# Optimization experiments

Hardware: AMD Instinct MI355X
Metric: run time of the kernel (lower is better)

The kernel has to match this reference:

```python
import jax, jax.numpy as jnp
import numpy as np

N_NODES = 100000
N_EDGES = 1600000
IN_CH, HID, OUT_CH = 256, 128, 40
NUM_LAYERS = 8
ALPHA = 0.5
THETA = 1.0


def setup_inputs() -> dict:
    key = jax.random.key(0)
    ks = jax.random.split(key, 8)
    x = jax.random.normal(ks[0], (N_NODES, IN_CH), dtype=jnp.float32)
    edge_index = jax.random.randint(ks[1], (2, N_EDGES), 0, N_NODES, dtype=jnp.int64)
    s1 = 1.0 / np.sqrt(IN_CH)
    s2 = 1.0 / np.sqrt(HID)
    lin1_w = jax.random.uniform(ks[2], (IN_CH, HID), jnp.float32, -s1, s1)
    lin1_b = jax.random.uniform(ks[3], (HID,), jnp.float32, -s1, s1)
    conv_ws = jax.random.uniform(ks[4], (NUM_LAYERS, HID, HID), jnp.float32, -s2, s2)
    lin2_w = jax.random.uniform(ks[5], (HID, OUT_CH), jnp.float32, -s2, s2)
    lin2_b = jax.random.uniform(ks[6], (OUT_CH,), jnp.float32, -s2, s2)
    return {"x": x, "edge_index": edge_index, "lin1_w": lin1_w, "lin1_b": lin1_b,
            "conv_ws": conv_ws, "lin2_w": lin2_w, "lin2_b": lin2_b}


def reference(x, edge_index, lin1_w, lin1_b, conv_ws, lin2_w, lin2_b):
    # Eval mode: dropout is identity. GCN2Conv with shared_weights=True:
    #   h_agg = A_hat @ h ; h = (1-alpha)*h_agg + alpha*x0
    #   out  = (1-beta)*h + beta*(h @ W_l), beta = log(theta/l + 1)
    n = x.shape[0]
    loops = jnp.arange(n, dtype=edge_index.dtype)
    row = jnp.concatenate([edge_index[0], loops])  # source
    col = jnp.concatenate([edge_index[1], loops])  # target (aggregation)
    deg = jax.ops.segment_sum(jnp.ones(row.shape[0], dtype=x.dtype), col, num_segments=n)
    dinv = jnp.where(deg > 0, deg ** -0.5, 0.0)
    enorm = dinv[row] * dinv[col]  # symmetric GCN normalization, [E+N]

    h = jax.nn.relu(x @ lin1_w + lin1_b)  # [N, HID]
    x0 = h
    for l in range(NUM_LAYERS):
        beta = float(np.log(THETA / (l + 1) + 1.0))
        agg = jax.ops.segment_sum(h[row] * enorm[:, None], col, num_segments=n)
        hc = (1.0 - ALPHA) * agg + ALPHA * x0
        h = jax.nn.relu((1.0 - beta) * hc + beta * (hc @ conv_ws[l]))
    out = h @ lin2_w + lin2_b
    return jax.nn.log_softmax(out, axis=1)
```

## Files before the change

kernel.cpp:

```cpp
#include <hip/hip_runtime.h>
#include <math.h>

#define NN 100000
#define NE 1600000
#define HID 128
#define INCH 256
#define OUTC 40
#define NLAYERS 8
#define NBUCK 391
#define EPB 4096
#define CAP 6144
#define LW 136

typedef __attribute__((ext_vector_type(8))) short bf16x8;
typedef __attribute__((ext_vector_type(4))) float f32x4;
typedef __attribute__((ext_vector_type(2))) float f32x2;

static __device__ inline unsigned short f2bf(float f) {
  unsigned u = __float_as_uint(f);
  unsigned r = (u + 0x7fff + ((u >> 16) & 1)) >> 16;
  return (unsigned short)r;
}
static __device__ inline float bflo(unsigned u) { return __uint_as_float(u << 16); }
static __device__ inline float bfhi(unsigned u) { return __uint_as_float(u & 0xffff0000u); }
static __device__ inline unsigned char f2fp8(float f) {
  return (unsigned char)(__builtin_amdgcn_cvt_pk_fp8_f32(f, f, 0, false) & 0xff);
}


static __global__ void k_zerob(int* __restrict__ bcnt, int* __restrict__ dbin) {
  int i = blockIdx.x * 256 + threadIdx.x;
  if (i < NBUCK) bcnt[i] = 0;
  if (i < 64) dbin[i] = 0;
}

static __global__ __launch_bounds__(256) void k_bhist(const int* __restrict__ ei,
                                                      int* __restrict__ bcnt) {
  __shared__ int lh[NBUCK + 1];
  int t = threadIdx.x;
  for (int i = t; i <= NBUCK; i += 256) lh[i] = 0;
  __syncthreads();
  int e0 = blockIdx.x * EPB;
  for (int k = t; k < EPB; k += 256) {
    int e = e0 + k;
    if (e < NE) atomicAdd(&lh[ei[NE + e] >> 8], 1);
  }
  __syncthreads();
  for (int i = t; i < NBUCK; i += 256)
    if (lh[i]) atomicAdd(&bcnt[i], lh[i]);
}

static __global__ void k_bscan(const int* __restrict__ bcnt, int* __restrict__ boffs,
                               int* __restrict__ bcur, int* __restrict__ offs) {
  __shared__ int sd[512];
  int t = threadIdx.x;
  sd[t] = (t < NBUCK) ? bcnt[t] : 0;
  __syncthreads();
  for (int d = 1; d < 512; d <<= 1) {
    int v = (t >= d) ? sd[t - d] : 0;
    __syncthreads();
    sd[t] += v;
    __syncthreads();
  }
  if (t < NBUCK) {
    boffs[t + 1] = sd[t];
    bcur[t] = sd[t] - bcnt[t];
  }
  if (t == 0) { boffs[0] = 0; offs[NN] = NE; }
}

static __global__ __launch_bounds__(256) void k_sortA(const int* __restrict__ ei,
                                                      int* __restrict__ bcur,
                                                      int2* __restrict__ stage) {
  __shared__ int lsrc[EPB], ldst[EPB];
  __shared__ int lh[NBUCK + 1], lbase[NBUCK + 1], lcur[NBUCK + 1];
  int t = threadIdx.x;
  int e0 = blockIdx.x * EPB;
  for (int k = t; k < EPB; k += 256) {
    int e = e0 + k;
    lsrc[k] = (e < NE) ? ei[e] : -1;
    ldst[k] = (e < NE) ? ei[NE + e] : -1;
  }
  for (int i = t; i <= NBUCK; i += 256) lh[i] = 0;
  __syncthreads();
  for (int k = t; k < EPB; k += 256)
    if (ldst[k] >= 0) atomicAdd(&lh[ldst[k] >> 8], 1);
  __syncthreads();
  for (int i = t; i < NBUCK; i += 256) {
    int c = lh[i];
    lbase[i] = c ? atomicAdd(&bcur[i], c) : 0;
    lcur[i] = 0;
  }
  __syncthreads();
  for (int k = t; k < EPB; k += 256) {
    int d = ldst[k];
    if (d >= 0) {
      int bu = d >> 8;
      int r = atomicAdd(&lcur[bu], 1);
      stage[lbase[bu] + r] = make_int2(lsrc[k], d);
    }
  }
}

static __global__ __launch_bounds__(256) void k_degs(
    const int2* __restrict__ stage, const int* __restrict__ boffs,
    int* __restrict__ offs, float* __restrict__ dinv, int* __restrict__ cursor,
    int* __restrict__ deg, int* __restrict__ dbin) {
  __shared__ int lcnt[256];
  __shared__ int sd[256];
  __shared__ int lhd[64];
  int b = blockIdx.x, t = threadIdx.x;
  int sb = boffs[b], se = boffs[b + 1];
  int cntb = se - sb;
  int nb0 = b << 8;
  lcnt[t] = 0;
  if (t < 64) lhd[t] = 0;
  __syncthreads();
  for (int k = t; k < cntb; k += 256) atomicAdd(&lcnt[stage[sb + k].y - nb0], 1);
  __syncthreads();
  int v = lcnt[t];
  sd[t] = v;
  __syncthreads();
  for (int d = 1; d < 256; d <<= 1) {
    int u = (t >= d) ? sd[t - d] : 0;
    __syncthreads();
    sd[t] += u;
    __syncthreads();
  }
  int n = nb0 + t;
  if (n < NN) {
    int o = sb + sd[t] - v;
    offs[n] = o;
    cursor[n] = o;
    dinv[n] = rsqrtf((float)(v + 1));
    deg[n] = v;
    int bin = 63 - (v > 63 ? 63 : v);
    atomicAdd(&lhd[bin], 1);
  }
  __syncthreads();
  if (t < 64 && lhd[t]) atomicAdd(&dbin[t], lhd[t]);
}

static __global__ void k_dscan(const int* __restrict__ dbin, int* __restrict__ dcur) {
  __shared__ int sd[64];
  int t = threadIdx.x;
  sd[t] = dbin[t];
  __syncthreads();
  if (t == 0) {
    int a = 0;
    for (int i = 0; i < 64; ++i) { int v = sd[i]; sd[i] = a; a += v; }
  }
  __syncthreads();
  dcur[t] = sd[t];
}

static __global__ __launch_bounds__(256) void k_perm(const int* __restrict__ deg,
                                                     int* __restrict__ dcur,
                                                     int* __restrict__ perm,
                                                     int* __restrict__ inv) {
  __shared__ int lh[64], lbase[64], lcur[64];
  int t = threadIdx.x;
  int n = blockIdx.x * 256 + t;
  if (t < 64) { lh[t] = 0; lcur[t] = 0; }
  __syncthreads();
  int bin = 0;
  if (n < NN) {
    int d = deg[n];
    bin = 63 - (d > 63 ? 63 : d);
    atomicAdd(&lh[bin], 1);
  }
  __syncthreads();
  if (t < 64) lbase[t] = lh[t] ? atomicAdd(&dcur[t], lh[t]) : 0;
  __syncthreads();
  if (n < NN) {
    int r = atomicAdd(&lcur[bin], 1);
    int pos = lbase[bin] + r;
    perm[pos] = n;
    inv[n] = pos;
  }
}

static __global__ __launch_bounds__(256) void k_passB2(
    const int2* __restrict__ stage, const int* __restrict__ boffs,
    const int* __restrict__ offs, const float* __restrict__ dinv,
    const int* __restrict__ inv, int* __restrict__ cursor, int2* __restrict__ edata) {
  __shared__ int2 lbuf[CAP];
  __shared__ int lcur[256];
  int b = blockIdx.x, t = threadIdx.x;
  int sb = boffs[b], se = boffs[b + 1];
  int cntb = se - sb;
  int nb0 = b << 8;
  if (cntb <= CAP) {
    if (nb0 + t < NN) lcur[t] = offs[nb0 + t] - sb;
    __syncthreads();
    for (int k = t; k < cntb; k += 256) {
      int2 sd_ = stage[sb + k];
      float w = dinv[sd_.x] * dinv[sd_.y];
      int p = atomicAdd(&lcur[sd_.y - nb0], 1);
      lbuf[p] = make_int2(inv[sd_.x], __float_as_int(w));
    }
    __syncthreads();
    for (int k = t; k < cntb; k += 256) edata[sb + k] = lbuf[k];
  } else {
    for (int k = t; k < cntb; k += 256) {
      int2 sd_ = stage[sb + k];
      float w = dinv[sd_.x] * dinv[sd_.y];
      int p = atomicAdd(&cursor[sd_.y], 1);
      edata[p] = make_int2(inv[sd_.x], __float_as_int(w));
    }
  }
}

static __global__ void k_cvtall(const float* __restrict__ W1, const float* __restrict__ CW,
                                const float* __restrict__ W2, unsigned short* __restrict__ wt1,
                                unsigned short* __restrict__ wtl,
                                unsigned short* __restrict__ wt2) {
  int idx = blockIdx.x * 256 + threadIdx.x;
  if (idx < INCH * HID) {
    int k = idx >> 7, n = idx & 127;
    wt1[(size_t)n * INCH + k] = f2bf(W1[idx]);
  } else if (idx < INCH * HID + NLAYERS * HID * HID) {
    int r = idx - INCH * HID;
    int l = r >> 14, rem = r & 16383;
    int k = rem >> 7, n = rem & 127;
    float beta = logf(1.0f / (float)(l + 1) + 1.0f);
    float v = beta * CW[r];
    if (k == n) v += 1.0f - beta;
    wtl[(size_t)l * HID * HID + n * HID + k] = f2bf(v);
  } else if (idx < INCH * HID + NLAYERS * HID * HID + 48 * HID) {
    int r = idx - INCH * HID - NLAYERS * HID * HID;
    int n = r >> 7, k = r & 127;
    wt2[r] = (n < OUTC) ? f2bf(W2[(size_t)k * OUTC + n]) : 0;
  }
}

__global__ __launch_bounds__(256, 4) void k_lin1(
    const float* __restrict__ A32, const unsigned short* __restrict__ Wt16,
    const float* __restrict__ bias, const int* __restrict__ inv,
    unsigned short* __restrict__ C16, unsigned char* __restrict__ C8, int M) {
  __shared__ unsigned short lds[64 * LW];
  __shared__ int ldst[64];
  const int tid = threadIdx.x;
  const int lane = tid & 63;
  const int wid = tid >> 6;
  const int j = lane & 15, g = lane >> 4;
  const int rq = (wid >> 1) * 32;
  const int colbase = (wid & 1) * 64;
  const int m0 = blockIdx.x * 64;

  if (tid < 64) {
    int r = m0 + tid;
    ldst[tid] = inv[r >= M ? M - 1 : r];
  }

  f32x4 acc[2][4];
  const f32x4 zero = {0.f, 0.f, 0.f, 0.f};
#pragma unroll
  for (int rt = 0; rt < 2; ++rt)
#pragma unroll
    for (int c = 0; c < 4; ++c) acc[rt][c] = zero;

#pragma unroll 1
  for (int kc = 0; kc < 2; ++kc) {
    __syncthreads();
#pragma unroll
    for (int u = 0; u < 4; ++u) {
      int idx = u * 256 + tid;
      int row = idx >> 4, ch = idx & 15;
      int grow = m0 + row;
      if (grow >= M) grow = M - 1;
      const float* p = A32 + (size_t)grow * INCH + kc * 128 + ch * 8;
      float4 u0 = *(const float4*)p;
      float4 u1 = *(const float4*)(p + 4);
      bf16x8 v;
      v[0] = (short)f2bf(u0.x); v[1] = (short)f2bf(u0.y);
      v[2] = (short)f2bf(u0.z); v[3] = (short)f2bf(u0.w);
      v[4] = (short)f2bf(u1.x); v[5] = (short)f2bf(u1.y);
      v[6] = (short)f2bf(u1.z); v[7] = (short)f2bf(u1.w);
      *(bf16x8*)&lds[row * LW + ch * 8] = v;
    }
    __syncthreads();
    bf16x8 bfrag[4][4];
#pragma unroll
    for (int c = 0; c < 4; ++c)
#pragma unroll
      for (int s = 0; s < 4; ++s)
        bfrag[c][s] = *(const bf16x8*)(Wt16 + (size_t)(colbase + 16 * c + j) * INCH +
                                       kc * 128 + 32 * s + 8 * g);
#pragma unroll
    for (int rt = 0; rt < 2; ++rt) {
      bf16x8 af[4];
#pragma unroll
      for (int s = 0; s < 4; ++s)
        af[s] = *(const bf16x8*)&lds[(rq + rt * 16 + j) * LW + 32 * s + 8 * g];
#pragma unroll
      for (int s = 0; s < 4; ++s)
#pragma unroll
        for (int c = 0; c < 4; ++c)
          acc[rt][c] =
              __builtin_amdgcn_mfma_f32_16x16x32_bf16(af[s], bfrag[c][s], acc[rt][c], 0, 0, 0);
    }
  }

  __syncthreads();
#pragma unroll
  for (int rt = 0; rt < 2; ++rt)
#pragma unroll
    for (int i = 0; i < 4; ++i) {
      const int row = rq + rt * 16 + 4 * g + i;
#pragma unroll
      for (int c = 0; c < 4; ++c) {
        const int col = colbase + 16 * c + j;
        lds[row * LW + col] = f2bf(fmaxf(acc[rt][c][i] + bias[col], 0.f));
      }
    }
  __syncthreads();

  {
    const int r = tid >> 2, q = tid & 3;
    if (m0 + r < M) {
      const unsigned short* src = &lds[r * LW + q * 32];
      uint4 v0 = *(const uint4*)(src);
      uint4 v1 = *(const uint4*)(src + 8);
      uint4 v2 = *(const uint4*)(src + 16);
      uint4 v3 = *(const uint4*)(src + 24);
      size_t base = (size_t)ldst[r] * HID + q * 32;
      *(uint4*)(C16 + base) = v0;
      *(uint4*)(C16 + base + 8) = v1;
      *(uint4*)(C16 + base + 16) = v2;
      *(uint4*)(C16 + base + 24) = v3;
      unsigned char q8[32];
      const unsigned* uu0 = (const unsigned*)&v0;
      const unsigned* uu1 = (const unsigned*)&v1;
      const unsigned* uu2 = (const unsigned*)&v2;
      const unsigned* uu3 = (const unsigned*)&v3;
#pragma unroll
      for (int s = 0; s < 4; ++s) {
        q8[2 * s] = f2fp8(bflo(uu0[s]));       q8[2 * s + 1] = f2fp8(bfhi(uu0[s]));
        q8[8 + 2 * s] = f2fp8(bflo(uu1[s]));   q8[9 + 2 * s] = f2fp8(bfhi(uu1[s]));
        q8[16 + 2 * s] = f2fp8(bflo(uu2[s]));  q8[17 + 2 * s] = f2fp8(bfhi(uu2[s]));
        q8[24 + 2 * s] = f2fp8(bflo(uu3[s]));  q8[25 + 2 * s] = f2fp8(bfhi(uu3[s]));
      }
      *(uint4*)(C8 + base) = *(const uint4*)&q8[0];
      *(uint4*)(C8 + base + 16) = *(const uint4*)&q8[16];
    }
  }
}

#define ACCD(U, O, W)                                                   \
  {                                                                     \
    f32x2 lo_ = __builtin_amdgcn_cvt_pk_f32_fp8((U), false);            \
    f32x2 hi_ = __builtin_amdgcn_cvt_pk_f32_fp8((U), true);             \
    acc[(O) + 0] = fmaf((W), lo_.x, acc[(O) + 0]);                      \
    acc[(O) + 1] = fmaf((W), lo_.y, acc[(O) + 1]);                      \
    acc[(O) + 2] = fmaf((W), hi_.x, acc[(O) + 2]);                      \
    acc[(O) + 3] = fmaf((W), hi_.y, acc[(O) + 3]);                      \
  }

#define ACCROW8(VA, VB, W)                                              \
  ACCD((VA).x, 0, W) ACCD((VA).y, 4, W) ACCD((VA).z, 8, W) ACCD((VA).w, 12, W) \
  ACCD((VB).x, 16, W) ACCD((VB).y, 20, W) ACCD((VB).z, 24, W) ACCD((VB).w, 28, W)

__global__ __launch_bounds__(256) void k_fused(
    const unsigned char* __restrict__ h8, const unsigned short* __restrict__ x016,
    const float* __restrict__ dinv, const int* __restrict__ offs,
    const int2* __restrict__ edata, const int* __restrict__ perm,
    const unsigned short* __restrict__ Wt16, unsigned char* __restrict__ h8out,
    unsigned short* __restrict__ C16, int M) {
  __shared__ unsigned short lds[64 * LW];
  const int tid = threadIdx.x;
  const int m0 = blockIdx.x * 64;
  const int newid = m0 + (tid >> 2);
  const int cq = (tid & 3) * 32;

  float acc[32];
#pragma unroll
  for (int q = 0; q < 32; ++q) acc[q] = 0.f;

  unsigned short q16[32];
  if (newid < M) {
    const int node = perm[newid];
    int b = offs[node], e = offs[node + 1];
    float dn = dinv[node];
    {
      const unsigned char* p = h8 + (size_t)newid * HID + cq;
      uint4 s0 = *(const uint4*)p, s1 = *(const uint4*)(p + 16);
      float w = dn * dn;
      ACCROW8(s0, s1, w)
    }
    int i = b;
    int2 n0, n1;
    if (i + 3 < e) { n0 = edata[i]; n1 = edata[i + 1]; }
    for (; i + 3 < e; i += 2) {
      int2 c0 = n0, c1 = n1;
      n0 = edata[i + 2];
      n1 = edata[i + 3];
      const unsigned char* p0 = h8 + (size_t)c0.x * HID + cq;
      const unsigned char* p1 = h8 + (size_t)c1.x * HID + cq;
      uint4 r0 = *(const uint4*)p0, r1 = *(const uint4*)(p0 + 16);
      uint4 r2 = *(const uint4*)p1, r3 = *(const uint4*)(p1 + 16);
      float w0 = __int_as_float(c0.y), w1 = __int_as_float(c1.y);
      ACCROW8(r0, r1, w0)
      ACCROW8(r2, r3, w1)
    }
    for (; i < e; ++i) {
      int2 e0 = edata[i];
      const unsigned char* p0 = h8 + (size_t)e0.x * HID + cq;
      uint4 r0 = *(const uint4*)p0, r1 = *(const uint4*)(p0 + 16);
      float w0 = __int_as_float(e0.y);
      ACCROW8(r0, r1, w0)
    }
    const unsigned short* px = x016 + (size_t)newid * HID + cq;
    uint4 xa = *(const uint4*)px, xb = *(const uint4*)(px + 8);
    uint4 xc = *(const uint4*)(px + 16), xd = *(const uint4*)(px + 24);
    float xo[32];
#define UNP8(V, O)                                                     \
    xo[(O) + 0] = bflo((V).x); xo[(O) + 1] = bfhi((V).x);              \
    xo[(O) + 2] = bflo((V).y); xo[(O) + 3] = bfhi((V).y);              \
    xo[(O) + 4] = bflo((V).z); xo[(O) + 5] = bfhi((V).z);              \
    xo[(O) + 6] = bflo((V).w); xo[(O) + 7] = bfhi((V).w);
    UNP8(xa, 0) UNP8(xb, 8) UNP8(xc, 16) UNP8(xd, 24)
#undef UNP8
#pragma unroll
    for (int q = 0; q < 32; ++q) q16[q] = f2bf(0.5f * acc[q] + 0.5f * xo[q]);
  } else {
#pragma unroll
    for (int q = 0; q < 32; ++q) q16[q] = 0;
  }
  {
    unsigned short* lrow = &lds[(tid >> 2) * LW + cq];
    *(uint4*)(lrow) = *(const uint4*)&q16[0];
    *(uint4*)(lrow + 8) = *(const uint4*)&q16[8];
    *(uint4*)(lrow + 16) = *(const uint4*)&q16[16];
    *(uint4*)(lrow + 24) = *(const uint4*)&q16[24];
  }
  __syncthreads();

  const int lane = tid & 63;
  const int wid = tid >> 6;
  const int rq = (wid >> 1) * 32;
  const int colbase = (wid & 1) * 64;
  const int j = lane & 15, g = lane >> 4;

  bf16x8 bfrag[4][4];
#pragma unroll
  for (int c = 0; c < 4; ++c)
#pragma unroll
    for (int s = 0; s < 4; ++s)
      bfrag[c][s] =
          *(const bf16x8*)(Wt16 + (size_t)(colbase + 16 * c + j) * HID + 32 * s + 8 * g);

  const f32x4 zero = {0.f, 0.f, 0.f, 0.f};
#pragma unroll
  for (int rt = 0; rt < 2; ++rt) {
    bf16x8 af[4];
#pragma unroll
    for (int s = 0; s < 4; ++s)
      af[s] = *(const bf16x8*)&lds[(rq + rt * 16 + j) * LW + 32 * s + 8 * g];
    f32x4 a2[4] = {zero, zero, zero, zero};
#pragma unroll
    for (int s = 0; s < 4; ++s)
#pragma unroll
      for (int c = 0; c < 4; ++c)
        a2[c] = __builtin_amdgcn_mfma_f32_16x16x32_bf16(af[s], bfrag[c][s], a2[c], 0, 0, 0);
#pragma unroll
    for (int i = 0; i < 4; ++i) {
      const int rr = m0 + rq + rt * 16 + 4 * g + i;
      if (rr >= M) continue;
#pragma unroll
      for (int c = 0; c < 4; ++c) {
        const int col = colbase + 16 * c + j;
        float z = fmaxf(a2[c][i], 0.f);
        h8out[(size_t)rr * HID + col] = f2fp8(z);
        if (C16) C16[(size_t)rr * HID + col] = f2bf(z);
      }
    }
  }
}

static __global__ __launch_bounds__(256, 3) void k_mlin2(
    const unsigned short* __restrict__ h16, const unsigned short* __restrict__ Wt2,
    const float* __restrict__ b2, const int* __restrict__ perm,
    float* __restrict__ out) {
  __shared__ unsigned short lds[128 * LW];
  const int tid = threadIdx.x;
  const int lane = tid & 63;
  const int wid = tid >> 6;
  const int j = lane & 15, g = lane >> 4;
  const int m0 = blockIdx.x * 128;

  bf16x8 bfrag[3][4];
#pragma unroll
  for (int c = 0; c < 3; ++c)
#pragma unroll
    for (int s = 0; s < 4; ++s)
      bfrag[c][s] = *(const bf16x8*)(Wt2 + (size_t)(16 * c + j) * HID + 32 * s + 8 * g);

  float bb[3];
#pragma unroll
  for (int c = 0; c < 3; ++c) {
    int col = 16 * c + j;
    bb[c] = (col < OUTC) ? b2[col] : -1e30f;
  }

#pragma unroll 2
  for (int i = 0; i < 8; ++i) {
    int idx = i * 256 + tid;
    int row = idx >> 4, ch = idx & 15;
    int grow = m0 + row;
    if (grow >= NN) grow = NN - 1;
    *(bf16x8*)&lds[row * LW + ch * 8] =
        *(const bf16x8*)(h16 + (size_t)grow * HID + ch * 8);
  }
  __syncthreads();

  const f32x4 zero = {0.f, 0.f, 0.f, 0.f};
#pragma unroll
  for (int rt = 0; rt < 2; ++rt) {
    bf16x8 af[4];
#pragma unroll
    for (int s = 0; s < 4; ++s)
      af[s] = *(const bf16x8*)&lds[(wid * 32 + rt * 16 + j) * LW + 32 * s + 8 * g];
    f32x4 acc[3] = {zero, zero, zero};
#pragma unroll
    for (int s = 0; s < 4; ++s)
#pragma unroll
      for (int c = 0; c < 3; ++c)
        acc[c] = __builtin_amdgcn_mfma_f32_16x16x32_bf16(af[s], bfrag[c][s], acc[c], 0, 0, 0);

#pragma unroll
    for (int i = 0; i < 4; ++i) {
      const int rr = m0 + wid * 32 + rt * 16 + 4 * g + i;
      if (rr >= NN) continue;
      float z0 = acc[0][i] + bb[0];
      float z1 = acc[1][i] + bb[1];
      float z2 = acc[2][i] + bb[2];
      float m = fmaxf(fmaxf(z0, z1), z2);
      m = fmaxf(m, __shfl_xor(m, 1));
      m = fmaxf(m, __shfl_xor(m, 2));
      m = fmaxf(m, __shfl_xor(m, 4));
      m = fmaxf(m, __shfl_xor(m, 8));
      float sum = __expf(z0 - m) + __expf(z1 - m) + __expf(z2 - m);
      sum += __shfl_xor(sum, 1);
      sum += __shfl_xor(sum, 2);
      sum += __shfl_xor(sum, 4);
      sum += __shfl_xor(sum, 8);
      float ls = m + logf(sum);
      int orig = perm[rr];
      out[(size_t)orig * OUTC + j] = z0 - ls;
      out[(size_t)orig * OUTC + 16 + j] = z1 - ls;
      if (j < 8) out[(size_t)orig * OUTC + 32 + j] = z2 - ls;
    }
  }
}

extern "C" void kernel_launch(void* const* d_in, const int* in_sizes, int n_in,
                              void* d_out, int out_size, void* d_ws, size_t ws_size,
                              hipStream_t stream) {
  const float* x  = (const float*)d_in[0];
  const int*   ei = (const int*)d_in[1];
  const float* w1 = (const float*)d_in[2];
  const float* b1 = (const float*)d_in[3];
  const float* cw = (const float*)d_in[4];
  const float* w2 = (const float*)d_in[5];
  const float* b2 = (const float*)d_in[6];
  float* out = (float*)d_out;

  char* ws = (char*)d_ws;
  size_t o = 0;
  auto carve = [&](size_t bytes) {
    void* p = ws + o;
    o = (o + bytes + 255) & ~(size_t)255;
    return p;
  };
  float* dinv   = (float*)carve((size_t)NN * 4);
  int*   offs   = (int*)carve((size_t)(NN + 1) * 4);
  int*   cursor = (int*)carve((size_t)NN * 4);
  int*   bcnt   = (int*)carve((size_t)NBUCK * 4);
  int*   boffs  = (int*)carve((size_t)(NBUCK + 1) * 4);
  int*   bcur   = (int*)carve((size_t)NBUCK * 4);
  int*   deg    = (int*)carve((size_t)NN * 4);
  int*   dbin   = (int*)carve(64 * 4);
  int*   dcur   = (int*)carve(64 * 4);
  int*   perm   = (int*)carve((size_t)NN * 4);
  int*   inv    = (int*)carve((size_t)NN * 4);
  int2*  stage  = (int2*)carve((size_t)NE * 8);
  int2*  edata  = (int2*)carve((size_t)NE * 8);
  unsigned short* x016 = (unsigned short*)carve((size_t)NN * HID * 2);
  unsigned short* hb16 = (unsigned short*)carve((size_t)NN * HID * 2);
  unsigned char*  h8A  = (unsigned char*)carve((size_t)NN * HID);
  unsigned char*  h8B  = (unsigned char*)carve((size_t)NN * HID);
  unsigned short* wt1  = (unsigned short*)carve((size_t)INCH * HID * 2);
  unsigned short* wtl  = (unsigned short*)carve((size_t)NLAYERS * HID * HID * 2);
  unsigned short* wt2  = (unsigned short*)carve((size_t)48 * HID * 2);
  (void)ws_size; (void)in_sizes; (void)n_in; (void)out_size;

  const int TB = 256;
  const int gEB = (NE + EPB - 1) / EPB;

  k_zerob<<<(NBUCK + 255) / 256, TB, 0, stream>>>(bcnt, dbin);
  k_bhist<<<gEB, TB, 0, stream>>>(ei, bcnt);
  k_bscan<<<1, 512, 0, stream>>>(bcnt, boffs, bcur, offs);
  k_sortA<<<gEB, TB, 0, stream>>>(ei, bcur, stage);
  k_degs<<<NBUCK, TB, 0, stream>>>(stage, boffs, offs, dinv, cursor, deg, dbin);
  k_dscan<<<1, 64, 0, stream>>>(dbin, dcur);
  k_perm<<<NBUCK, TB, 0, stream>>>(deg, dcur, perm, inv);
  k_passB2<<<NBUCK, TB, 0, stream>>>(stage, boffs, offs, dinv, inv, cursor, edata);

  const int cvtTotal = INCH * HID + NLAYERS * HID * HID + 48 * HID;
  k_cvtall<<<(cvtTotal + 255) / 256, 256, 0, stream>>>(w1, cw, w2, wt1, wtl, wt2);

  const int gF = (NN + 63) / 64;
  k_lin1<<<gF, 256, 0, stream>>>(x, wt1, b1, inv, x016, h8A, NN);

  const unsigned char* hin = h8A;
  unsigned char* hout = h8B;
  for (int l = 0; l < NLAYERS; ++l) {
    unsigned short* c16 = (l == NLAYERS - 1) ? hb16 : nullptr;
    k_fused<<<gF, 256, 0, stream>>>(hin, x016, dinv, offs, edata, perm,
                                    wtl + (size_t)l * HID * HID, hout, c16, NN);
    hin = hout;
    hout = (hout == h8A) ? h8B : h8A;
  }
  k_mlin2<<<(NN + 127) / 128, 256, 0, stream>>>(hb16, wt2, b2, perm, out);
}
```

Baseline: 562.2 us.

## Precompute per-node header in permuted order; shrink lin1 tile to 32 rows

Adds a kernel that builds a packed int4 header per permuted node (edge range begin/end and the self-loop weight dinv squared). Each of the eight fused layer kernels then does one coalesced 16-byte load instead of a perm lookup followed by scattered offs and dinv reads. Separately, k_lin1 now uses 32-row tiles with one row tile per wave, which doubles the grid and lowers LDS and register use for more occupancy. The cost is an extra small kernel launch and 1.6 MB of header storage, and lin1 reloads the weight fragments twice as often.

Measured after the change: 567.2 us. No clear change (+0.9%).

```diff
diff --git a/kernel.cpp b/kernel.cpp
--- a/kernel.cpp
+++ b/kernel.cpp
@@ -177,6 +177,16 @@
     int pos = lbase[bin] + r;
     perm[pos] = n;
     inv[n] = pos;
+  }
+}
+
+static __global__ void k_hdr(const int* __restrict__ perm, const int* __restrict__ offs,
+                             const float* __restrict__ dinv, int4* __restrict__ hdr) {
+  int i = blockIdx.x * 256 + threadIdx.x;
+  if (i < NN) {
+    int n = perm[i];
+    float d = dinv[n];
+    hdr[i] = make_int4(offs[n], offs[n + 1], __float_as_int(d * d), 0);
   }
 }
 
@@ -238,33 +248,31 @@
     const float* __restrict__ A32, const unsigned short* __restrict__ Wt16,
     const float* __restrict__ bias, const int* __restrict__ inv,
     unsigned short* __restrict__ C16, unsigned char* __restrict__ C8, int M) {
-  __shared__ unsigned short lds[64 * LW];
-  __shared__ int ldst[64];
+  __shared__ unsigned short lds[32 * LW];
+  __shared__ int ldst[32];
   const int tid = threadIdx.x;
   const int lane = tid & 63;
   const int wid = tid >> 6;
   const int j = lane & 15, g = lane >> 4;
-  const int rq = (wid >> 1) * 32;
+  const int rq = (wid >> 1) * 16;
   const int colbase = (wid & 1) * 64;
-  const int m0 = blockIdx.x * 64;
-
-  if (tid < 64) {
+  const int m0 = blockIdx.x * 32;
+
+  if (tid < 32) {
     int r = m0 + tid;
     ldst[tid] = inv[r >= M ? M - 1 : r];
   }
 
-  f32x4 acc[2][4];
+  f32x4 acc[4];
   const f32x4 zero = {0.f, 0.f, 0.f, 0.f};
 #pragma unroll
-  for (int rt = 0; rt < 2; ++rt)
-#pragma unroll
-    for (int c = 0; c < 4; ++c) acc[rt][c] = zero;
+  for (int c = 0; c < 4; ++c) acc[c] = zero;
 
 #pragma unroll 1
   for (int kc = 0; kc < 2; ++kc) {
     __syncthreads();
 #pragma unroll
-    for (int u = 0; u < 4; ++u) {
+    for (int u = 0; u < 2; ++u) {
       int idx = u * 256 + tid;
       int row = idx >> 4, ch = idx & 15;
       int grow = m0 + row;
@@ -287,62 +295,47 @@
       for (int s = 0; s < 4; ++s)
         bfrag[c][s] = *(const bf16x8*)(Wt16 + (size_t)(colbase + 16 * c + j) * INCH +
                                        kc * 128 + 32 * s + 8 * g);
-#pragma unroll
-    for (int rt = 0; rt < 2; ++rt) {
-      bf16x8 af[4];
-#pragma unroll
-      for (int s = 0; s < 4; ++s)
-        af[s] = *(const bf16x8*)&lds[(rq + rt * 16 + j) * LW + 32 * s + 8 * g];
-#pragma unroll
-      for (int s = 0; s < 4; ++s)
-#pragma unroll
-        for (int c = 0; c < 4; ++c)
-          acc[rt][c] =
-              __builtin_amdgcn_mfma_f32_16x16x32_bf16(af[s], bfrag[c][s], acc[rt][c], 0, 0, 0);
-    }
-  }
-
-  __syncthreads();
-#pragma unroll
-  for (int rt = 0; rt < 2; ++rt)
-#pragma unroll
-    for (int i = 0; i < 4; ++i) {
-      const int row = rq + rt * 16 + 4 * g + i;
-#pragma unroll
-      for (int c = 0; c < 4; ++c) {
-        const int col = colbase + 16 * c + j;
-        lds[row * LW + col] = f2bf(fmaxf(acc[rt][c][i] + bias[col], 0.f));
-      }
-    }
+    bf16x8 af[4];
+#pragma unroll
+    for (int s = 0; s < 4; ++s)
+      af[s] = *(const bf16x8*)&lds[(rq + j) * LW + 32 * s + 8 * g];
+#pragma unroll
+    for (int s = 0; s < 4; ++s)
+#pragma unroll
+      for (int c = 0; c < 4; ++c)
+        acc[c] = __builtin_amdgcn_mfma_f32_16x16x32_bf16(af[s], bfrag[c][s], acc[c], 0, 0, 0);
+  }
+
+  __syncthreads();
+#pragma unroll
+  for (int i = 0; i < 4; ++i) {
+    const int row = rq + 4 * g + i;
+#pragma unroll
+    for (int c = 0; c < 4; ++c) {
+      const int col = colbase + 16 * c + j;
+      lds[row * LW + col] = f2bf(fmaxf(acc[c][i] + bias[col], 0.f));
+    }
+  }
   __syncthreads();
 
   {
-    const int r = tid >> 2, q = tid & 3;
+    const int r = tid >> 3, q = tid & 7;
     if (m0 + r < M) {
-      const unsigned short* src = &lds[r * LW + q * 32];
+      const unsigned short* src = &lds[r * LW + q * 16];
       uint4 v0 = *(const uint4*)(src);
       uint4 v1 = *(const uint4*)(src + 8);
-      uint4 v2 = *(const uint4*)(src + 16);
-      uint4 v3 = *(const uint4*)(src + 24);
-      size_t base = (size_t)ldst[r] * HID + q * 32;
+      size_t base = (size_t)ldst[r] * HID + q * 16;
       *(uint4*)(C16 + base) = v0;
       *(uint4*)(C16 + base + 8) = v1;
-      *(uint4*)(C16 + base + 16) = v2;
-      *(uint4*)(C16 + base + 24) = v3;
-      unsigned char q8[32];
+      unsigned char q8[16];
       const unsigned* uu0 = (const unsigned*)&v0;
       const unsigned* uu1 = (const unsigned*)&v1;
-      const unsigned* uu2 = (const unsigned*)&v2;
-      const unsigned* uu3 = (const unsigned*)&v3;
 #pragma unroll
       for (int s = 0; s < 4; ++s) {
-        q8[2 * s] = f2fp8(bflo(uu0[s]));       q8[2 * s + 1] = f2fp8(bfhi(uu0[s]));
-        q8[8 + 2 * s] = f2fp8(bflo(uu1[s]));   q8[9 + 2 * s] = f2fp8(bfhi(uu1[s]));
-        q8[16 + 2 * s] = f2fp8(bflo(uu2[s]));  q8[17 + 2 * s] = f2fp8(bfhi(uu2[s]));
-        q8[24 + 2 * s] = f2fp8(bflo(uu3[s]));  q8[25 + 2 * s] = f2fp8(bfhi(uu3[s]));
+        q8[2 * s] = f2fp8(bflo(uu0[s]));      q8[2 * s + 1] = f2fp8(bfhi(uu0[s]));
+        q8[8 + 2 * s] = f2fp8(bflo(uu1[s]));  q8[9 + 2 * s] = f2fp8(bfhi(uu1[s]));
       }
       *(uint4*)(C8 + base) = *(const uint4*)&q8[0];
-      *(uint4*)(C8 + base + 16) = *(const uint4*)&q8[16];
     }
   }
 }
@@ -363,8 +356,7 @@
 
 __global__ __launch_bounds__(256) void k_fused(
     const unsigned char* __restrict__ h8, const unsigned short* __restrict__ x016,
-    const float* __restrict__ dinv, const int* __restrict__ offs,
-    const int2* __restrict__ edata, const int* __restrict__ perm,
+    const int4* __restrict__ hdr, const int2* __restrict__ edata,
     const unsigned short* __restrict__ Wt16, unsigned char* __restrict__ h8out,
     unsigned short* __restrict__ C16, int M) {
   __shared__ unsigned short lds[64 * LW];
@@ -379,13 +371,12 @@
 
   unsigned short q16[32];
   if (newid < M) {
-    const int node = perm[newid];
-    int b = offs[node], e = offs[node + 1];
-    float dn = dinv[node];
+    const int4 hd = hdr[newid];
+    const int b = hd.x, e = hd.y;
     {
       const unsigned char* p = h8 + (size_t)newid * HID + cq;
       uint4 s0 = *(const uint4*)p, s1 = *(const uint4*)(p + 16);
-      float w = dn * dn;
+      float w = __int_as_float(hd.z);
       ACCROW8(s0, s1, w)
     }
     int i = b;
@@ -584,6 +575,7 @@
   int*   dcur   = (int*)carve(64 * 4);
   int*   perm   = (int*)carve((size_t)NN * 4);
   int*   inv    = (int*)carve((size_t)NN * 4);
+  int4*  hdr    = (int4*)carve((size_t)NN * 16);
   int2*  stage  = (int2*)carve((size_t)NE * 8);
   int2*  edata  = (int2*)carve((size_t)NE * 8);
   unsigned short* x016 = (unsigned short*)carve((size_t)NN * HID * 2);
@@ -605,19 +597,20 @@
   k_degs<<<NBUCK, TB, 0, stream>>>(stage, boffs, offs, dinv, cursor, deg, dbin);
   k_dscan<<<1, 64, 0, stream>>>(dbin, dcur);
   k_perm<<<NBUCK, TB, 0, stream>>>(deg, dcur, perm, inv);
+  k_hdr<<<NBUCK, TB, 0, stream>>>(perm, offs, dinv, hdr);
   k_passB2<<<NBUCK, TB, 0, stream>>>(stage, boffs, offs, dinv, inv, cursor, edata);
 
   const int cvtTotal = INCH * HID + NLAYERS * HID * HID + 48 * HID;
   k_cvtall<<<(cvtTotal + 255) / 256, 256, 0, stream>>>(w1, cw, w2, wt1, wtl, wt2);
 
+  k_lin1<<<(NN + 31) / 32, 256, 0, stream>>>(x, wt1, b1, inv, x016, h8A, NN);
+
   const int gF = (NN + 63) / 64;
-  k_lin1<<<gF, 256, 0, stream>>>(x, wt1, b1, inv, x016, h8A, NN);
-
   const unsigned char* hin = h8A;
   unsigned char* hout = h8B;
   for (int l = 0; l < NLAYERS; ++l) {
     unsigned short* c16 = (l == NLAYERS - 1) ? hb16 : nullptr;
-    k_fused<<<gF, 256, 0, stream>>>(hin, x016, dinv, offs, edata, perm,
+    k_fused<<<gF, 256, 0, stream>>>(hin, x016, hdr, edata,
                                     wtl + (size_t)l * HID * HID, hout, c16, NN);
     hin = hout;
     hout = (hout == h8A) ? h8B : h8A;
```
